# Kernel optimization log

Hardware: AMD Instinct MI355X
Metric: run time of the kernel (lower is better)

Reference implementation:

```python
import jax, jax.numpy as jnp
import numpy as np

N_NODES = 100000
N_EDGES = 1600000
IN_CH = 128
HID = 256
OUT_CH = 128
N_GRAPHS = 2048


def setup_inputs() -> dict:
    key = jax.random.key(0)
    ks = jax.random.split(key, 12)
    x = jax.random.normal(ks[0], (N_NODES, IN_CH), dtype=jnp.float32)
    edge_index = jax.random.randint(ks[1], (2, N_EDGES), 0, N_NODES, dtype=jnp.int32)
    batch = jnp.sort(jax.random.randint(ks[2], (N_NODES,), 0, N_GRAPHS, dtype=jnp.int32))
    s = lambda k, shp, fan: jax.random.normal(k, shp, dtype=jnp.float32) / np.sqrt(fan)
    params = {
        # SAGEConv1: lin_l (applied to aggregated neighbors, has bias) and lin_r (root)
        "W1l": s(ks[3], (IN_CH, HID), IN_CH), "b1": jnp.zeros((HID,), jnp.float32),
        "W1r": s(ks[4], (IN_CH, HID), IN_CH),
        # SAGEConv2
        "W2l": s(ks[5], (HID, HID), HID), "b2": jnp.zeros((HID,), jnp.float32),
        "W2r": s(ks[6], (HID, HID), HID),
        # MLP head
        "W3": s(ks[7], (HID, HID), HID), "b3": jnp.zeros((HID,), jnp.float32),
        "W4": s(ks[8], (HID, OUT_CH), HID), "b4": jnp.zeros((OUT_CH,), jnp.float32),
    }
    return {"x": x, "edge_index": edge_index, "batch": batch, **params}


def _sage_conv(x, src, dst, Wl, bl, Wr, num_nodes):
    # PyG SAGEConv (aggr='mean'): out_i = Wl @ mean_{j->i} x_j + bl + Wr @ x_i
    agg = jax.ops.segment_sum(x[src], dst, num_segments=num_nodes)  # [N, C]
    cnt = jax.ops.segment_sum(jnp.ones((src.shape[0],), x.dtype), dst, num_segments=num_nodes)
    mean = agg / jnp.maximum(cnt, 1.0)[:, None]
    return mean @ Wl + bl + x @ Wr


def reference(x, edge_index, batch, W1l, b1, W1r, W2l, b2, W2r, W3, b3, W4, b4):
    src, dst = edge_index[0], edge_index[1]
    h = jax.nn.relu(_sage_conv(x, src, dst, W1l, b1, W1r, N_NODES))
    # dropout is identity in eval mode
    h = jax.nn.relu(_sage_conv(h, src, dst, W2l, b2, W2r, N_NODES))
    # global_mean_pool over graphs
    psum = jax.ops.segment_sum(h, batch, num_segments=N_GRAPHS)  # [G, HID]
    gcnt = jax.ops.segment_sum(jnp.ones((h.shape[0],), h.dtype), batch, num_segments=N_GRAPHS)
    pooled = psum / jnp.maximum(gcnt, 1.0)[:, None]
    # MLP head
    hidden = jax.nn.relu(pooled @ W3 + b3)
    return hidden @ W4 + b4  # [G, OUT_CH]
```

## Files before the change

kernel.cpp:

```cpp
#include <hip/hip_runtime.h>

#define N_NODES 100000
#define N_EDGES 1600000
#define IN_CH 128
#define HID 256
#define OUT_CH 128
#define N_GRAPHS 2048

#define NBUK 391
#define CHUNK 8192

typedef __attribute__((ext_vector_type(8))) short bf16x8;
typedef __attribute__((ext_vector_type(4))) float f32x4;
typedef __attribute__((ext_vector_type(2))) float f32x2;

__device__ inline unsigned short f2b(float f) {
    unsigned int u = __builtin_bit_cast(unsigned int, f);
    u = (u + 0x7FFF + ((u >> 16) & 1)) >> 16;
    return (unsigned short)u;
}
__device__ inline float b2f(unsigned short h) {
    unsigned int u = (unsigned int)h << 16;
    return __builtin_bit_cast(float, u);
}

#define GLOAD_LDS16(gsrc, ldst)                                                   \
    __builtin_amdgcn_global_load_lds(                                             \
        (const __attribute__((address_space(1))) void*)(gsrc),                    \
        (__attribute__((address_space(3))) void*)(ldst), 16, 0, 0)

#define SCAN_ITEMS 8
#define SCAN_TILE (256 * SCAN_ITEMS)

__global__ void scan1_k(const int* __restrict__ in, int* __restrict__ out,
                        int* __restrict__ bsums, int n) {
    __shared__ int wsum[4];
    int base = blockIdx.x * SCAN_TILE + (int)threadIdx.x * SCAN_ITEMS;
    int v[SCAN_ITEMS];
    int s = 0;
    #pragma unroll
    for (int i = 0; i < SCAN_ITEMS; ++i) {
        v[i] = (base + i < n) ? in[base + i] : 0;
        s += v[i];
    }
    int lane = threadIdx.x & 63, wid = threadIdx.x >> 6;
    int incl = s;
    #pragma unroll
    for (int off = 1; off < 64; off <<= 1) {
        int t = __shfl_up(incl, off, 64);
        if (lane >= off) incl += t;
    }
    if (lane == 63) wsum[wid] = incl;
    __syncthreads();
    int wprefix = 0;
    #pragma unroll
    for (int w = 0; w < 4; ++w)
        if (w < wid) wprefix += wsum[w];
    int run = wprefix + incl - s;
    #pragma unroll
    for (int i = 0; i < SCAN_ITEMS; ++i) {
        if (base + i < n) out[base + i] = run;
        run += v[i];
    }
    if (threadIdx.x == 255) bsums[blockIdx.x] = wprefix + incl;
}

__global__ void scan2_k(int* __restrict__ bsums, int nb, int* __restrict__ total) {
    __shared__ int wsum[4];
    int v = ((int)threadIdx.x < nb) ? bsums[threadIdx.x] : 0;
    int lane = threadIdx.x & 63, wid = threadIdx.x >> 6;
    int incl = v;
    #pragma unroll
    for (int off = 1; off < 64; off <<= 1) {
        int t = __shfl_up(incl, off, 64);
        if (lane >= off) incl += t;
    }
    if (lane == 63) wsum[wid] = incl;
    __syncthreads();
    int wprefix = 0;
    #pragma unroll
    for (int w = 0; w < 4; ++w)
        if (w < wid) wprefix += wsum[w];
    if ((int)threadIdx.x < nb) bsums[threadIdx.x] = wprefix + incl - v;
    if (threadIdx.x == 255) *total = wprefix + incl;
}

__global__ void bucket_count_k(const int* __restrict__ dst, int* __restrict__ bcnt, int E) {
    __shared__ int cnt[NBUK];
    int tid = threadIdx.x;
    for (int i = tid; i < NBUK; i += 256) cnt[i] = 0;
    __syncthreads();
    int e0 = blockIdx.x * CHUNK;
    int eend = min(e0 + CHUNK, E);
    for (int e = e0 + tid; e < eend; e += 256)
        atomicAdd(&cnt[dst[e] >> 8], 1);
    __syncthreads();
    for (int i = tid; i < NBUK; i += 256)
        if (cnt[i]) atomicAdd(&bcnt[i], cnt[i]);
}

__global__ void bin_scatter_k(const int* __restrict__ src, const int* __restrict__ dst,
                              const int* __restrict__ bbase, int* __restrict__ bcur,
                              uint2* __restrict__ staging, int E) {
    __shared__ int cnt[NBUK];
    __shared__ int gbase[NBUK];
    int tid = threadIdx.x;
    for (int i = tid; i < NBUK; i += 256) cnt[i] = 0;
    __syncthreads();
    int e0 = blockIdx.x * CHUNK;
    int eend = min(e0 + CHUNK, E);
    for (int e = e0 + tid; e < eend; e += 256)
        atomicAdd(&cnt[dst[e] >> 8], 1);
    __syncthreads();
    for (int i = tid; i < NBUK; i += 256) {
        int c = cnt[i];
        gbase[i] = c ? (bbase[i] + atomicAdd(&bcur[i], c)) : 0;
        cnt[i] = 0;
    }
    __syncthreads();
    for (int e = e0 + tid; e < eend; e += 256) {
        int d = dst[e];
        int b = d >> 8;
        int l = atomicAdd(&cnt[b], 1);
        uint2 p; p.x = (unsigned)src[e]; p.y = (unsigned)d;
        staging[(size_t)gbase[b] + l] = p;
    }
}

__global__ void csr_build_k(const uint2* __restrict__ staging, const int* __restrict__ bbase,
                            int* __restrict__ row_ofs, int* __restrict__ csr) {
    __shared__ int ldeg[256];
    __shared__ int lofs[256];
    __shared__ int wsum[4];
    int b = blockIdx.x, tid = threadIdx.x;
    int base = bbase[b];
    int cnt = bbase[b + 1] - base;
    ldeg[tid] = 0;
    __syncthreads();
    const uint2* sp = staging + base;
    for (int i = tid; i < cnt; i += 256)
        atomicAdd(&ldeg[sp[i].y & 255], 1);
    __syncthreads();
    int v = ldeg[tid];
    int lane = tid & 63, wid = tid >> 6;
    int incl = v;
    #pragma unroll
    for (int off = 1; off < 64; off <<= 1) {
        int t = __shfl_up(incl, off, 64);
        if (lane >= off) incl += t;
    }
    if (lane == 63) wsum[wid] = incl;
    __syncthreads();
    int wprefix = 0;
    #pragma unroll
    for (int w = 0; w < 4; ++w)
        if (w < wid) wprefix += wsum[w];
    int excl = wprefix + incl - v;
    lofs[tid] = excl;
    int node = b * 256 + tid;
    if (node < N_NODES) row_ofs[node] = base + excl;
    if (b == NBUK - 1 && tid == 0) row_ofs[N_NODES] = N_EDGES;
    ldeg[tid] = 0;
    __syncthreads();
    for (int i = tid; i < cnt; i += 256) {
        uint2 p = sp[i];
        int d = (int)p.y & 255;
        int pos = atomicAdd(&ldeg[d], 1);
        csr[base + lofs[d] + pos] = (int)p.x;
    }
}

__global__ void gofs_search_k(const int* __restrict__ batch, int* __restrict__ gofs,
                              int n, int G) {
    int g = blockIdx.x * blockDim.x + threadIdx.x;
    if (g > G) return;
    if (g == G) { gofs[G] = n; return; }
    int lo = 0, hi = n;
    while (lo < hi) {
        int mid = (lo + hi) >> 1;
        if (batch[mid] < g) lo = mid + 1; else hi = mid;
    }
    gofs[g] = lo;
}

__global__ void wt_concat_k(const float* __restrict__ Wl, const float* __restrict__ Wr,
                            unsigned short* __restrict__ out, int K1, int K2, int N) {
    int idx = blockIdx.x * blockDim.x + threadIdx.x;
    int KT = K1 + K2;
    if (idx >= N * KT) return;
    int n = idx / KT, k = idx % KT;
    float v = (k < K1) ? Wl[(size_t)k * N + n] : Wr[(size_t)(k - K1) * N + n];
    out[idx] = f2b(v);
}

__global__ void f2b8_k(const float* __restrict__ in, unsigned short* __restrict__ outb,
                       unsigned char* __restrict__ out8, size_t n8) {
    size_t i = (size_t)blockIdx.x * blockDim.x + threadIdx.x;
    if (i >= n8) return;
    float4 a = ((const float4*)in)[i * 2];
    float4 b = ((const float4*)in)[i * 2 + 1];
    unsigned short ob[8];
    ob[0] = f2b(a.x); ob[1] = f2b(a.y); ob[2] = f2b(a.z); ob[3] = f2b(a.w);
    ob[4] = f2b(b.x); ob[5] = f2b(b.y); ob[6] = f2b(b.z); ob[7] = f2b(b.w);
    ((uint4*)outb)[i] = *(const uint4*)ob;
    int w0 = 0, w1 = 0;
    w0 = __builtin_amdgcn_cvt_pk_fp8_f32(a.x, a.y, w0, false);
    w0 = __builtin_amdgcn_cvt_pk_fp8_f32(a.z, a.w, w0, true);
    w1 = __builtin_amdgcn_cvt_pk_fp8_f32(b.x, b.y, w1, false);
    w1 = __builtin_amdgcn_cvt_pk_fp8_f32(b.z, b.w, w1, true);
    uint2 o8; o8.x = (unsigned int)w0; o8.y = (unsigned int)w1;
    ((uint2*)out8)[i] = o8;
}

template <int C>
__global__ void agg_f8_k(const unsigned char* __restrict__ X8, const int* __restrict__ row_ofs,
                         const int* __restrict__ csr, unsigned short* __restrict__ out, int n) {
    constexpr int GL = C / 16;
    constexpr int NG = 64 / GL;
    int w = (int)((blockIdx.x * blockDim.x + threadIdx.x) >> 6);
    int lane = threadIdx.x & 63;
    if (w >= n) return;
    int g = lane / GL, il = lane % GL;
    int s = row_ofs[w], e = row_ofs[w + 1];
    float a[16];
    #pragma unroll
    for (int t = 0; t < 16; ++t) a[t] = 0.f;

    int j = s + g;
    for (; j + NG < e; j += 2 * NG) {
        int i0 = csr[j], i1 = csr[j + NG];
        uint4 r0 = *(const uint4*)&X8[(size_t)i0 * C + il * 16];
        uint4 r1 = *(const uint4*)&X8[(size_t)i1 * C + il * 16];
        const unsigned int* q0 = (const unsigned int*)&r0;
        const unsigned int* q1 = (const unsigned int*)&r1;
        #pragma unroll
        for (int t = 0; t < 4; ++t) {
            f32x2 lo = __builtin_amdgcn_cvt_pk_f32_fp8(q0[t], false);
            f32x2 hi = __builtin_amdgcn_cvt_pk_f32_fp8(q0[t], true);
            a[t * 4 + 0] += lo.x; a[t * 4 + 1] += lo.y;
            a[t * 4 + 2] += hi.x; a[t * 4 + 3] += hi.y;
        }
        #pragma unroll
        for (int t = 0; t < 4; ++t) {
            f32x2 lo = __builtin_amdgcn_cvt_pk_f32_fp8(q1[t], false);
            f32x2 hi = __builtin_amdgcn_cvt_pk_f32_fp8(q1[t], true);
            a[t * 4 + 0] += lo.x; a[t * 4 + 1] += lo.y;
            a[t * 4 + 2] += hi.x; a[t * 4 + 3] += hi.y;
        }
    }
    if (j < e) {
        int i0 = csr[j];
        uint4 r0 = *(const uint4*)&X8[(size_t)i0 * C + il * 16];
        const unsigned int* q0 = (const unsigned int*)&r0;
        #pragma unroll
        for (int t = 0; t < 4; ++t) {
            f32x2 lo = __builtin_amdgcn_cvt_pk_f32_fp8(q0[t], false);
            f32x2 hi = __builtin_amdgcn_cvt_pk_f32_fp8(q0[t], true);
            a[t * 4 + 0] += lo.x; a[t * 4 + 1] += lo.y;
            a[t * 4 + 2] += hi.x; a[t * 4 + 3] += hi.y;
        }
    }

    #pragma unroll
    for (int m = GL; m < 64; m <<= 1)
        #pragma unroll
        for (int t = 0; t < 16; ++t) a[t] += __shfl_xor(a[t], m, 64);

    if (g == 0) {
        float inv = 1.0f / (float)max(e - s, 1);
        uint4 o0, o1;
        unsigned short* p0 = (unsigned short*)&o0;
        unsigned short* p1 = (unsigned short*)&o1;
        #pragma unroll
        for (int t = 0; t < 8; ++t) p0[t] = f2b(a[t] * inv);
        #pragma unroll
        for (int t = 0; t < 8; ++t) p1[t] = f2b(a[8 + t] * inv);
        *(uint4*)&out[(size_t)w * C + il * 16] = o0;
        *(uint4*)&out[(size_t)w * C + il * 16 + 8] = o1;
    }
}

__global__ void pool_mean_k(const unsigned short* __restrict__ H, const int* __restrict__ gofs,
                            float* __restrict__ pooled, int G) {
    int g = (int)((blockIdx.x * blockDim.x + threadIdx.x) >> 6);
    int lane = threadIdx.x & 63;
    if (g >= G) return;
    int s = gofs[g], e = gofs[g + 1];
    float a0 = 0.f, a1 = 0.f, a2 = 0.f, a3 = 0.f;
    for (int r = s; r < e; ++r) {
        ushort4 t = ((const ushort4*)(H + (size_t)r * HID))[lane];
        a0 += b2f(t.x); a1 += b2f(t.y); a2 += b2f(t.z); a3 += b2f(t.w);
    }
    float inv = 1.0f / (float)max(e - s, 1);
    float4 o; o.x = a0 * inv; o.y = a1 * inv; o.z = a2 * inv; o.w = a3 * inv;
    ((float4*)(pooled + (size_t)g * HID))[lane] = o;
}

__launch_bounds__(256)
__global__ void mfma_gemm_k(const unsigned short* __restrict__ A1, int K1,
                            const unsigned short* __restrict__ A2, int K2,
                            const unsigned short* __restrict__ Bt,
                            const float* __restrict__ bias, int M, int Nfull,
                            void* __restrict__ Cptr, unsigned char* __restrict__ f8out,
                            int c_bf16, int do_relu) {
    __shared__ short ldsA[2 * 4096];
    __shared__ short ldsB[2 * 4096];
    int tid = threadIdx.x, lane = tid & 63;
    int wid = tid >> 6, wm = wid >> 1, wn = wid & 1;
    int row0 = blockIdx.x * 128, col0 = blockIdx.y * 128;
    int q = lane >> 4, l15 = lane & 15;
    int KT = K1 + K2;
    int nk = KT / 32;

    int rr = tid >> 2;
    int c8 = (tid & 3) * 8;
    int dof = wid * 512;

    auto stage = [&](int t) {
        int kt = t * 32;
        const unsigned short* Asrc; int kk, Ks;
        if (kt < K1) { Asrc = A1; kk = kt; Ks = K1; }
        else         { Asrc = A2; kk = kt - K1; Ks = K2; }
        short* bA = ldsA + (t & 1) * 4096;
        short* bB = ldsB + (t & 1) * 4096;
        #pragma unroll
        for (int h = 0; h < 2; ++h) {
            int r = h * 64 + rr;
            int gr = min(row0 + r, M - 1);
            GLOAD_LDS16(Asrc + (size_t)gr * Ks + kk + c8, bA + h * 2048 + dof);
            GLOAD_LDS16(Bt + (size_t)(col0 + r) * KT + kt + c8, bB + h * 2048 + dof);
        }
    };

    f32x4 acc[4][4] = {};

    stage(0);
    stage(1);

    for (int t = 0; t < nk; ++t) {
        if (t == nk - 1) asm volatile("s_waitcnt vmcnt(0)" ::: "memory");
        else             asm volatile("s_waitcnt vmcnt(4)" ::: "memory");
        asm volatile("s_barrier" ::: "memory");

        const short* bA = ldsA + (t & 1) * 4096;
        const short* bB = ldsB + (t & 1) * 4096;
        bf16x8 af[4], bfr[4];
        #pragma unroll
        for (int i = 0; i < 4; ++i)
            af[i] = *(const bf16x8*)&bA[(wm * 64 + i * 16 + l15) * 32 + q * 8];
        #pragma unroll
        for (int j = 0; j < 4; ++j)
            bfr[j] = *(const bf16x8*)&bB[(wn * 64 + j * 16 + l15) * 32 + q * 8];
        #pragma unroll
        for (int i = 0; i < 4; ++i)
            #pragma unroll
            for (int j = 0; j < 4; ++j)
                acc[i][j] = __builtin_amdgcn_mfma_f32_16x16x32_bf16(af[i], bfr[j], acc[i][j], 0, 0, 0);

        asm volatile("s_barrier" ::: "memory");
        if (t + 2 < nk) stage(t + 2);
    }

    #pragma unroll
    for (int i = 0; i < 4; ++i) {
        #pragma unroll
        for (int reg = 0; reg < 4; ++reg) {
            int r = row0 + wm * 64 + i * 16 + q * 4 + reg;
            if (r < M) {
                #pragma unroll
                for (int j = 0; j < 4; ++j) {
                    int cc = col0 + wn * 64 + j * 16 + l15;
                    float v = acc[i][j][reg] + bias[cc];
                    if (do_relu) v = fmaxf(v, 0.f);
                    if (c_bf16) ((unsigned short*)Cptr)[(size_t)r * Nfull + cc] = f2b(v);
                    else        ((float*)Cptr)[(size_t)r * Nfull + cc] = v;
                    if (f8out) {
                        int w8 = __builtin_amdgcn_cvt_pk_fp8_f32(v, v, 0, false);
                        f8out[(size_t)r * Nfull + cc] = (unsigned char)(w8 & 0xFF);
                    }
                }
            }
        }
    }
}

#define BM_ 64
#define BK_ 16

template <int BN_>
__launch_bounds__(256)
__global__ void gemm2_k(const float* __restrict__ A1, const float* __restrict__ B1, int K1,
                        const float* __restrict__ bias, float* __restrict__ C,
                        int M, int N, int do_relu) {
    constexpr int TCOLS = BN_ / 8;
    constexpr int TROWS = 256 / TCOLS;
    constexpr int TM = BM_ / TROWS;
    __shared__ float As[BK_][BM_ + 4];
    __shared__ float Bs[BK_][BN_ + 4];
    int tid = threadIdx.x;
    int row0 = blockIdx.x * BM_;
    int col0 = blockIdx.y * BN_;
    int tx = tid % TCOLS, ty = tid / TCOLS;

    float acc[TM][8];
    #pragma unroll
    for (int i = 0; i < TM; ++i)
        #pragma unroll
        for (int j = 0; j < 8; ++j) acc[i][j] = 0.f;

    int ar = tid >> 2;
    int ak = (tid & 3) * 4;

    for (int kt = 0; kt < K1; kt += BK_) {
        {
            int r = row0 + ar;
            int rc = min(r, M - 1);
            float4 v = *(const float4*)(A1 + (size_t)rc * K1 + kt + ak);
            As[ak + 0][ar] = v.x;
            As[ak + 1][ar] = v.y;
            As[ak + 2][ar] = v.z;
            As[ak + 3][ar] = v.w;
        }
        {
            #pragma unroll
            for (int h = 0; h < BN_ / 64; ++h) {
                int idx = h * 256 + tid;
                int kr = idx / (BN_ / 4);
                int c4 = idx % (BN_ / 4);
                float4 v = *(const float4*)(B1 + (size_t)(kt + kr) * N + col0 + c4 * 4);
                *(float4*)&Bs[kr][c4 * 4] = v;
            }
        }
        __syncthreads();

        #pragma unroll
        for (int k = 0; k < BK_; ++k) {
            float a[TM], b[8];
            #pragma unroll
            for (int v = 0; v < TM / 4; ++v)
                *(float4*)&a[v * 4] = *(const float4*)&As[k][ty * TM + v * 4];
            *(float4*)&b[0] = *(const float4*)&Bs[k][tx * 8];
            *(float4*)&b[4] = *(const float4*)&Bs[k][tx * 8 + 4];
            #pragma unroll
            for (int i = 0; i < TM; ++i)
                #pragma unroll
                for (int j = 0; j < 8; ++j) acc[i][j] = fmaf(a[i], b[j], acc[i][j]);
        }
        __syncthreads();
    }

    float bv[8];
    #pragma unroll
    for (int j = 0; j < 8; ++j) bv[j] = bias[col0 + tx * 8 + j];
    #pragma unroll
    for (int i = 0; i < TM; ++i) {
        int r = row0 + ty * TM + i;
        if (r < M) {
            float* cp = C + (size_t)r * N + col0 + tx * 8;
            float o[8];
            #pragma unroll
            for (int j = 0; j < 8; ++j) {
                float v = acc[i][j] + bv[j];
                o[j] = do_relu ? fmaxf(v, 0.f) : v;
            }
            *(float4*)(cp + 0) = *(float4*)&o[0];
            *(float4*)(cp + 4) = *(float4*)&o[4];
        }
    }
}

extern "C" void kernel_launch(void* const* d_in, const int* in_sizes, int n_in,
                              void* d_out, int out_size, void* d_ws, size_t ws_size,
                              hipStream_t stream) {
    const float* x    = (const float*)d_in[0];
    const int*   ei   = (const int*)d_in[1];
    const int*   batch= (const int*)d_in[2];
    const float* W1l  = (const float*)d_in[3];
    const float* b1   = (const float*)d_in[4];
    const float* W1r  = (const float*)d_in[5];
    const float* W2l  = (const float*)d_in[6];
    const float* b2   = (const float*)d_in[7];
    const float* W2r  = (const float*)d_in[8];
    const float* W3   = (const float*)d_in[9];
    const float* b3   = (const float*)d_in[10];
    const float* W4   = (const float*)d_in[11];
    const float* b4   = (const float*)d_in[12];
    float* out = (float*)d_out;

    const int N = N_NODES, E = N_EDGES, G = N_GRAPHS;
    const int* src = ei;
    const int* dst = ei + E;

    char* ws = (char*)d_ws;
    size_t off = 0;
    auto alloc = [&](size_t bytes) -> char* {
        off = (off + 255) & ~(size_t)255;
        char* p = ws + off;
        off += bytes;
        return p;
    };
    int* bcnt    = (int*)alloc((size_t)NBUK * 4);
    int* bcur    = (int*)alloc((size_t)NBUK * 4);
    size_t zero_span = (size_t)((char*)(bcur + NBUK) - (char*)bcnt);
    int* bbase   = (int*)alloc((size_t)(NBUK + 1) * 4);
    int* bsums   = (int*)alloc(256 * 4);
    int* row_ofs = (int*)alloc((size_t)(N + 1) * 4);
    int* gofs    = (int*)alloc((size_t)(G + 1) * 4);
    uint2* staging = (uint2*)alloc((size_t)E * 8);
    int* csr     = (int*)alloc((size_t)E * 4);
    unsigned short* xb    = (unsigned short*)alloc((size_t)N * IN_CH * 2);
    unsigned short* mean1 = (unsigned short*)alloc((size_t)N * IN_CH * 2);
    unsigned short* h1    = (unsigned short*)alloc((size_t)N * HID * 2);
    unsigned short* mean2 = (unsigned short*)alloc((size_t)N * HID * 2);
    unsigned short* h2    = xb;
    unsigned char*  x8    = (unsigned char*)alloc((size_t)N * IN_CH);
    unsigned char*  h1f8  = (unsigned char*)alloc((size_t)N * HID);
    unsigned short* W1T   = (unsigned short*)alloc((size_t)HID * (IN_CH + IN_CH) * 2);
    unsigned short* W2T   = (unsigned short*)alloc((size_t)HID * (HID + HID) * 2);
    float* pooled = (float*)alloc((size_t)G * HID * 4);
    float* hidden = (float*)alloc((size_t)G * HID * 4);
    (void)ws_size;

    hipMemsetAsync(bcnt, 0, zero_span, stream);

    const int EB = (E + CHUNK - 1) / CHUNK;
    bucket_count_k<<<EB, 256, 0, stream>>>(dst, bcnt, E);
    scan1_k<<<1, 256, 0, stream>>>(bcnt, bbase, bsums, NBUK);
    scan2_k<<<1, 256, 0, stream>>>(bsums, 1, bbase + NBUK);
    bin_scatter_k<<<EB, 256, 0, stream>>>(src, dst, bbase, bcur, staging, E);
    csr_build_k<<<NBUK, 256, 0, stream>>>(staging, bbase, row_ofs, csr);

    gofs_search_k<<<(G + 256) / 256, 256, 0, stream>>>(batch, gofs, N, G);

    wt_concat_k<<<(HID * 2 * IN_CH + 255) / 256, 256, 0, stream>>>(W1l, W1r, W1T, IN_CH, IN_CH, HID);
    wt_concat_k<<<(HID * 2 * HID + 255) / 256, 256, 0, stream>>>(W2l, W2r, W2T, HID, HID, HID);
    f2b8_k<<<(int)(((size_t)N * IN_CH / 8 + 255) / 256), 256, 0, stream>>>(
        x, xb, x8, (size_t)N * IN_CH / 8);

    const int MB = (N + 127) / 128;

    agg_f8_k<IN_CH><<<(N + 3) / 4, 256, 0, stream>>>(x8, row_ofs, csr, mean1, N);
    mfma_gemm_k<<<dim3(MB, HID / 128), 256, 0, stream>>>(
        mean1, IN_CH, xb, IN_CH, W1T, b1, N, HID, h1, h1f8, 1, 1);

    agg_f8_k<HID><<<(N + 3) / 4, 256, 0, stream>>>(h1f8, row_ofs, csr, mean2, N);
    mfma_gemm_k<<<dim3(MB, HID / 128), 256, 0, stream>>>(
        mean2, HID, h1, HID, W2T, b2, N, HID, h2, nullptr, 1, 1);

    pool_mean_k<<<(G + 3) / 4, 256, 0, stream>>>(h2, gofs, pooled, G);

    gemm2_k<HID><<<dim3(G / BM_, 1), 256, 0, stream>>>(
        pooled, W3, HID, b3, hidden, G, HID, 1);
    gemm2_k<OUT_CH><<<dim3(G / BM_, 1), 256, 0, stream>>>(
        hidden, W4, HID, b4, out, G, OUT_CH, 0);
}
```

Baseline: 554.7 us.

## Triple-buffer GEMM LDS staging and XOR-swizzle LDS layout

The MFMA GEMM kernel moves from double to triple buffering of its A/B tiles in LDS. This keeps two K-steps of global-to-LDS loads in flight while the current one is computed. It also applies an XOR swizzle on the 16-byte column chunk by row, applied both when staging and when reading fragments, to reduce LDS bank conflicts. In exchange the kernel uses 1.5x the LDS per block, which may lower occupancy.

```diff
diff --git a/kernel.cpp b/kernel.cpp
--- a/kernel.cpp
+++ b/kernel.cpp
@@ -303,8 +303,8 @@
                             const float* __restrict__ bias, int M, int Nfull,
                             void* __restrict__ Cptr, unsigned char* __restrict__ f8out,
                             int c_bf16, int do_relu) {
-    __shared__ short ldsA[2 * 4096];
-    __shared__ short ldsB[2 * 4096];
+    __shared__ short ldsA[3 * 4096];
+    __shared__ short ldsB[3 * 4096];
     int tid = threadIdx.x, lane = tid & 63;
     int wid = tid >> 6, wm = wid >> 1, wn = wid & 1;
     int row0 = blockIdx.x * 128, col0 = blockIdx.y * 128;
@@ -313,16 +313,14 @@
     int nk = KT / 32;
 
     int rr = tid >> 2;
-    int c8 = (tid & 3) * 8;
+    int c8 = ((tid & 3) ^ (rr & 3)) * 8;
     int dof = wid * 512;
 
-    auto stage = [&](int t) {
+    auto stage = [&](int t, short* bA, short* bB) {
         int kt = t * 32;
         const unsigned short* Asrc; int kk, Ks;
         if (kt < K1) { Asrc = A1; kk = kt; Ks = K1; }
         else         { Asrc = A2; kk = kt - K1; Ks = K2; }
-        short* bA = ldsA + (t & 1) * 4096;
-        short* bB = ldsB + (t & 1) * 4096;
         #pragma unroll
         for (int h = 0; h < 2; ++h) {
             int r = h * 64 + rr;
@@ -334,23 +332,30 @@
 
     f32x4 acc[4][4] = {};
 
-    stage(0);
-    stage(1);
-
+    stage(0, ldsA, ldsB);
+    stage(1, ldsA + 4096, ldsB + 4096);
+    stage(2, ldsA + 8192, ldsB + 8192);
+
+    int bi = 0;
     for (int t = 0; t < nk; ++t) {
-        if (t == nk - 1) asm volatile("s_waitcnt vmcnt(0)" ::: "memory");
-        else             asm volatile("s_waitcnt vmcnt(4)" ::: "memory");
+        if (t + 2 < nk)      asm volatile("s_waitcnt vmcnt(8)" ::: "memory");
+        else if (t + 1 < nk) asm volatile("s_waitcnt vmcnt(4)" ::: "memory");
+        else                 asm volatile("s_waitcnt vmcnt(0)" ::: "memory");
         asm volatile("s_barrier" ::: "memory");
 
-        const short* bA = ldsA + (t & 1) * 4096;
-        const short* bB = ldsB + (t & 1) * 4096;
+        short* bA = ldsA + bi * 4096;
+        short* bB = ldsB + bi * 4096;
         bf16x8 af[4], bfr[4];
         #pragma unroll
-        for (int i = 0; i < 4; ++i)
-            af[i] = *(const bf16x8*)&bA[(wm * 64 + i * 16 + l15) * 32 + q * 8];
-        #pragma unroll
-        for (int j = 0; j < 4; ++j)
-            bfr[j] = *(const bf16x8*)&bB[(wn * 64 + j * 16 + l15) * 32 + q * 8];
+        for (int i = 0; i < 4; ++i) {
+            int r = wm * 64 + i * 16 + l15;
+            af[i] = *(const bf16x8*)&bA[r * 32 + (q ^ (r & 3)) * 8];
+        }
+        #pragma unroll
+        for (int j = 0; j < 4; ++j) {
+            int r = wn * 64 + j * 16 + l15;
+            bfr[j] = *(const bf16x8*)&bB[r * 32 + (q ^ (r & 3)) * 8];
+        }
         #pragma unroll
         for (int i = 0; i < 4; ++i)
             #pragma unroll
@@ -358,7 +363,8 @@
                 acc[i][j] = __builtin_amdgcn_mfma_f32_16x16x32_bf16(af[i], bfr[j], acc[i][j], 0, 0, 0);
 
         asm volatile("s_barrier" ::: "memory");
-        if (t + 2 < nk) stage(t + 2);
+        if (t + 3 < nk) stage(t + 3, bA, bB);
+        bi = (bi == 2) ? 0 : bi + 1;
     }
 
     #pragma unroll
```

Result: no change. 551.7 us (-0.5%).

## Enlarge SAGE GEMM tiles to 256x256 with 4-stage LDS pipeline

Applied to the files above, without the earlier changes.

The node-level MFMA GEMM now uses 512-thread blocks computing 256x256 tiles, which cover the full hidden width in one block column, so each A row is loaded once instead of twice. The LDS double buffer becomes a four-stage ring with three tiles in flight and one barrier per k-step. It also raises wave priority around the MFMA loop. This costs 128KB of LDS and a 32-tile accumulator per wave, which limits occupancy to about one block per CU and leaves only about 391 blocks in the grid.

```diff
diff --git a/kernel.cpp b/kernel.cpp
--- a/kernel.cpp
+++ b/kernel.cpp
@@ -296,24 +296,23 @@
     ((float4*)(pooled + (size_t)g * HID))[lane] = o;
 }
 
-__launch_bounds__(256)
+__launch_bounds__(512)
 __global__ void mfma_gemm_k(const unsigned short* __restrict__ A1, int K1,
                             const unsigned short* __restrict__ A2, int K2,
                             const unsigned short* __restrict__ Bt,
                             const float* __restrict__ bias, int M, int Nfull,
                             void* __restrict__ Cptr, unsigned char* __restrict__ f8out,
                             int c_bf16, int do_relu) {
-    __shared__ short ldsA[2 * 4096];
-    __shared__ short ldsB[2 * 4096];
+    __shared__ short lds[4 * 16384];
     int tid = threadIdx.x, lane = tid & 63;
-    int wid = tid >> 6, wm = wid >> 1, wn = wid & 1;
-    int row0 = blockIdx.x * 128, col0 = blockIdx.y * 128;
+    int wid = tid >> 6, wm = wid >> 2, wn = wid & 3;
+    int row0 = blockIdx.x * 256, col0 = blockIdx.y * 256;
     int q = lane >> 4, l15 = lane & 15;
     int KT = K1 + K2;
     int nk = KT / 32;
 
     int rr = tid >> 2;
-    int c8 = (tid & 3) * 8;
+    int ck = (tid & 3) * 8;
     int dof = wid * 512;
 
     auto stage = [&](int t) {
@@ -321,51 +320,53 @@
         const unsigned short* Asrc; int kk, Ks;
         if (kt < K1) { Asrc = A1; kk = kt; Ks = K1; }
         else         { Asrc = A2; kk = kt - K1; Ks = K2; }
-        short* bA = ldsA + (t & 1) * 4096;
-        short* bB = ldsB + (t & 1) * 4096;
+        short* bA = lds + (t & 3) * 16384;
+        short* bB = bA + 8192;
         #pragma unroll
         for (int h = 0; h < 2; ++h) {
-            int r = h * 64 + rr;
-            int gr = min(row0 + r, M - 1);
-            GLOAD_LDS16(Asrc + (size_t)gr * Ks + kk + c8, bA + h * 2048 + dof);
-            GLOAD_LDS16(Bt + (size_t)(col0 + r) * KT + kt + c8, bB + h * 2048 + dof);
+            int gr = min(row0 + h * 128 + rr, M - 1);
+            GLOAD_LDS16(Asrc + (size_t)gr * Ks + kk + ck, bA + h * 4096 + dof);
+            GLOAD_LDS16(Bt + (size_t)(col0 + h * 128 + rr) * KT + kt + ck, bB + h * 4096 + dof);
         }
     };
 
-    f32x4 acc[4][4] = {};
+    f32x4 acc[8][4] = {};
 
     stage(0);
     stage(1);
+    stage(2);
 
     for (int t = 0; t < nk; ++t) {
-        if (t == nk - 1) asm volatile("s_waitcnt vmcnt(0)" ::: "memory");
-        else             asm volatile("s_waitcnt vmcnt(4)" ::: "memory");
+        if (t + 2 < nk)      asm volatile("s_waitcnt vmcnt(8)" ::: "memory");
+        else if (t + 1 < nk) asm volatile("s_waitcnt vmcnt(4)" ::: "memory");
+        else                 asm volatile("s_waitcnt vmcnt(0)" ::: "memory");
         asm volatile("s_barrier" ::: "memory");
 
-        const short* bA = ldsA + (t & 1) * 4096;
-        const short* bB = ldsB + (t & 1) * 4096;
-        bf16x8 af[4], bfr[4];
-        #pragma unroll
-        for (int i = 0; i < 4; ++i)
-            af[i] = *(const bf16x8*)&bA[(wm * 64 + i * 16 + l15) * 32 + q * 8];
+        if (t + 3 < nk) stage(t + 3);
+
+        const short* bA = lds + (t & 3) * 16384;
+        const short* bB = bA + 8192;
+        bf16x8 af[8], bf[4];
+        #pragma unroll
+        for (int i = 0; i < 8; ++i)
+            af[i] = *(const bf16x8*)&bA[(wm * 128 + i * 16 + l15) * 32 + q * 8];
         #pragma unroll
         for (int j = 0; j < 4; ++j)
-            bfr[j] = *(const bf16x8*)&bB[(wn * 64 + j * 16 + l15) * 32 + q * 8];
-        #pragma unroll
-        for (int i = 0; i < 4; ++i)
+            bf[j] = *(const bf16x8*)&bB[(wn * 64 + j * 16 + l15) * 32 + q * 8];
+        __builtin_amdgcn_s_setprio(1);
+        #pragma unroll
+        for (int i = 0; i < 8; ++i)
             #pragma unroll
             for (int j = 0; j < 4; ++j)
-                acc[i][j] = __builtin_amdgcn_mfma_f32_16x16x32_bf16(af[i], bfr[j], acc[i][j], 0, 0, 0);
-
-        asm volatile("s_barrier" ::: "memory");
-        if (t + 2 < nk) stage(t + 2);
-    }
-
-    #pragma unroll
-    for (int i = 0; i < 4; ++i) {
+                acc[i][j] = __builtin_amdgcn_mfma_f32_16x16x32_bf16(af[i], bf[j], acc[i][j], 0, 0, 0);
+        __builtin_amdgcn_s_setprio(0);
+    }
+
+    #pragma unroll
+    for (int i = 0; i < 8; ++i) {
         #pragma unroll
         for (int reg = 0; reg < 4; ++reg) {
-            int r = row0 + wm * 64 + i * 16 + q * 4 + reg;
+            int r = row0 + wm * 128 + i * 16 + q * 4 + reg;
             if (r < M) {
                 #pragma unroll
                 for (int j = 0; j < 4; ++j) {
@@ -537,14 +538,14 @@
     f2b8_k<<<(int)(((size_t)N * IN_CH / 8 + 255) / 256), 256, 0, stream>>>(
         x, xb, x8, (size_t)N * IN_CH / 8);
 
-    const int MB = (N + 127) / 128;
+    const int MB256 = (N + 255) / 256;
 
     agg_f8_k<IN_CH><<<(N + 3) / 4, 256, 0, stream>>>(x8, row_ofs, csr, mean1, N);
-    mfma_gemm_k<<<dim3(MB, HID / 128), 256, 0, stream>>>(
+    mfma_gemm_k<<<dim3(MB256, HID / 256), 512, 0, stream>>>(
         mean1, IN_CH, xb, IN_CH, W1T, b1, N, HID, h1, h1f8, 1, 1);
 
     agg_f8_k<HID><<<(N + 3) / 4, 256, 0, stream>>>(h1f8, row_ofs, csr, mean2, N);
-    mfma_gemm_k<<<dim3(MB, HID / 128), 256, 0, stream>>>(
+    mfma_gemm_k<<<dim3(MB256, HID / 256), 512, 0, stream>>>(
         mean2, HID, h1, HID, W2T, b2, N, HID, h2, nullptr, 1, 1);
 
     pool_mean_k<<<(G + 3) / 4, 256, 0, stream>>>(h2, gofs, pooled, G);
```

Measured after the change: 565.8 us. 1.02x slower.
